# Kernel optimization log

Measured on AMD Instinct MI355X. Metric: run time of the kernel, lower is better.

Reference implementation:

```python
import jax, jax.numpy as jnp
import numpy as np

# ---- problem constants (match init_kwargs) ----
M, N, DV = 4096, 8192, 4   # checks, variables, column weight
SEED = 0
MAX_ITER = 10
ALPHA = 0.8
CLAMP = 20.0
BATCH = 256
PAD_BIG = 1.0e6


def _build_code():
    """Deterministic regular-column-weight LDPC pcm + padded adjacency (mirrors torch __init__)."""
    rng = np.random.default_rng(SEED)
    pcm = np.zeros((M, N), dtype=np.uint8)
    for v in range(N):
        checks = rng.choice(M, size=DV, replace=False)
        pcm[checks, v] = 1
    check_indices, var_indices = np.nonzero(pcm)  # row-major: sorted by check
    num_edges = len(check_indices)
    check_adj_lists = [[] for _ in range(M)]
    var_adj_lists = [[] for _ in range(N)]
    for e in range(num_edges):
        check_adj_lists[int(check_indices[e])].append(e)
        var_adj_lists[int(var_indices[e])].append(e)
    max_dc = max(len(a) for a in check_adj_lists)
    max_dv = max(len(a) for a in var_adj_lists)
    check_adj = np.zeros((M, max_dc), dtype=np.int64)
    check_mask = np.zeros((M, max_dc), dtype=np.float32)
    for c, adj in enumerate(check_adj_lists):
        for j, e in enumerate(adj):
            check_adj[c, j] = e
            check_mask[c, j] = 1.0
    var_adj = np.zeros((N, max_dv), dtype=np.int64)
    var_mask = np.zeros((N, max_dv), dtype=np.float32)
    for v, adj in enumerate(var_adj_lists):
        for j, e in enumerate(adj):
            var_adj[v, j] = e
            var_mask[v, j] = 1.0
    return pcm, check_indices, var_indices, check_adj, check_mask, var_adj, var_mask


def setup_inputs() -> dict:
    key = jax.random.key(0)
    k1, k2 = jax.random.split(key)
    pcm, _, var_idx, check_adj, check_mask, var_adj, var_mask = _build_code()
    syndrome = jax.random.randint(k1, (BATCH, M), 0, 2).astype(jnp.float32)
    channel_llr = jax.random.normal(k2, (BATCH, N), dtype=jnp.float32) * 2.0
    return {
        "syndrome": syndrome,
        "channel_llr": channel_llr,
        "var_adj": jnp.asarray(var_adj, jnp.int32),
        "var_adj_mask": jnp.asarray(var_mask),
        "check_adj": jnp.asarray(check_adj, jnp.int32),
        "check_adj_mask": jnp.asarray(check_mask),
        "var_idx": jnp.asarray(var_idx, jnp.int32),
        "pcm_dense": jnp.asarray(pcm, jnp.float32),
    }


def reference(syndrome, channel_llr, var_adj, var_adj_mask, check_adj, check_adj_mask, var_idx, pcm_dense):
    B = syndrome.shape[0]
    E = var_idx.shape[0]
    s_sign = 1.0 - 2.0 * syndrome                      # [B, m]
    flat_cidx = check_adj.reshape(-1)                  # [m*max_dc]; padded slots point to edge 0 with value 0

    def step(ctv, _):
        # variable-node update: gather check->var messages per variable
        var_total = jnp.sum(ctv[:, var_adj] * var_adj_mask, axis=2)           # [B, n]
        vtc = channel_llr[:, var_idx] + var_total[:, var_idx] - ctv           # [B, E]
        vtc = jnp.clip(vtc, -CLAMP, CLAMP)
        # check-node min-sum update
        vg = vtc[:, check_adj]                                                # [B, m, dc]
        signs = jnp.where(vg >= 0.0, 1.0, -1.0)                               # sign(0) -> +1, as in torch path
        signs_m = signs * check_adj_mask + (1.0 - check_adj_mask)             # padded -> +1
        total_sign = s_sign[:, :, None] * jnp.prod(signs_m, axis=2, keepdims=True)
        excl_sign = total_sign * signs_m                                      # divide == multiply for +/-1
        absv = jnp.abs(vg) + (1.0 - check_adj_mask) * PAD_BIG                 # [B, m, dc]
        neg_top2, _ = jax.lax.top_k(-absv, 2)                                 # two smallest magnitudes
        min1 = -neg_top2[..., 0:1]
        min2 = -neg_top2[..., 1:2]
        is_min = jnp.abs(absv - min1) < 1e-9
        excl_min = jnp.where(is_min, min2, min1)
        ctv_new = ALPHA * excl_sign * excl_min * check_adj_mask               # [B, m, dc]
        # scatter back to flat edge layout (each real edge written exactly once; padded values are 0)
        ctv = jnp.zeros((B, E), ctv.dtype).at[:, flat_cidx].add(ctv_new.reshape(B, -1))
        return ctv, None

    ctv0 = jnp.zeros((B, E), jnp.float32)
    ctv, _ = jax.lax.scan(step, ctv0, None, length=MAX_ITER)

    var_total = jnp.sum(ctv[:, var_adj] * var_adj_mask, axis=2)
    total_llr = channel_llr + var_total
    marginals = jax.nn.sigmoid(-total_llr)                                    # [B, n]
    hard_decision = (marginals > 0.5).astype(jnp.int32)
    syn_hat = jnp.mod(jnp.round(hard_decision.astype(jnp.float32) @ pcm_dense.T), 2.0)
    converged = jnp.sum(jnp.abs(syn_hat - syndrome), axis=1) < 0.5
    return marginals, hard_decision, converged
```

## Files before the change

kernel.cpp:

```cpp
#include <hip/hip_runtime.h>
#include <math.h>


#define BLOCK 1024
#define NV    8192
#define MC    4096
#define NE    32768
#define VPT   (NV / BLOCK)
#define CPT   (MC / BLOCK)
#define NITER 10
#define ALPHA 0.8f
#define CLAMP 20.0f
#define MSGW  40896
#define SGNB  0x80000000


__device__ __forceinline__ int pad_stride(int d) { return d + ((2 - (d & 3)) & 3); }

__global__ __launch_bounds__(BLOCK)
void setup_sort(const float* __restrict__ check_mask,
                const int*   __restrict__ check_adj,
                int max_dc, int* __restrict__ ws)
{
    __shared__ int hist[64], cbase[64], wsum[16];
    __shared__ int sdeg[MC];
    const int t = threadIdx.x;
    if (t < 64) hist[t] = 0;
    __syncthreads();
    int deg[CPT];
#pragma unroll
    for (int k = 0; k < CPT; ++k) {
        const int c = t + k * BLOCK;
        int d = 0;
        for (int j = 0; j < max_dc; ++j)
            d += (check_mask[(size_t)c * max_dc + j] != 0.0f) ? 1 : 0;
        deg[k] = d;
        atomicAdd(&hist[d & 63], 1);
    }
    __syncthreads();
    if (t == 0) {
        int s = 0;
        for (int i = 0; i < 64; ++i) { cbase[i] = s; s += hist[i]; }
    }
    __syncthreads();
#pragma unroll
    for (int k = 0; k < CPT; ++k) {
        const int pos = atomicAdd(&cbase[deg[k] & 63], 1);
        sdeg[pos]    = deg[k];
        ws[MC + pos] = t + k * BLOCK;
    }
    __syncthreads();
    int psz[CPT];
    int s = 0;
#pragma unroll
    for (int k = 0; k < CPT; ++k) {
        const int d = sdeg[4 * t + k];
        psz[k] = s;
        s += pad_stride(d);
    }
    const int lane = t & 63, wv = t >> 6;
    int run = s;
#pragma unroll
    for (int off = 1; off < 64; off <<= 1) {
        const int n = __shfl_up(run, off, 64);
        if (lane >= off) run += n;
    }
    if (lane == 63) wsum[wv] = run;
    __syncthreads();
    if (t == 0) {
        int acc = 0;
        for (int w = 0; w < 16; ++w) { const int v = wsum[w]; wsum[w] = acc; acc += v; }
    }
    __syncthreads();
    const int tb = wsum[wv] + (run - s);
#pragma unroll
    for (int k = 0; k < CPT; ++k) {
        const int i = 4 * t + k;
        ws[i] = ((tb + psz[k]) & 0xFFFF) | (sdeg[i] << 16);
    }
}

template<int D>
__device__ __forceinline__ void do_check_x(char* __restrict__ mb,
                                           int stB, int ssb, float pad)
{
    float x[D];
    constexpr int P = D / 2;
#pragma unroll
    for (int p = 0; p < P; ++p) {
        const float2 r = *(const float2*)(mb + stB + 8 * p);
        x[2 * p]     = r.x;
        x[2 * p + 1] = r.y;
    }
    if constexpr (D & 1)
        x[D - 1] = *(const float*)(mb + stB + 4 * (D - 1));

    float min1 = pad, min2 = pad;
    int sb = ssb;
#pragma unroll
    for (int j = 0; j < D; ++j) {
        sb ^= __float_as_int(x[j]);
        const float a = fabsf(x[j]);
        min2 = __builtin_amdgcn_fmed3f(min1, min2, a);
        min1 = fminf(min1, a);
    }
    const float vm1 = ALPHA * min1;
    const float vm2 = ALPHA * min2;
#pragma unroll
    for (int p = 0; p < P; ++p) {
        const int j0 = 2 * p, j1 = 2 * p + 1;
        const float m0 = (fabsf(fabsf(x[j0]) - min1) < 1e-9f) ? vm2 : vm1;
        const float m1 = (fabsf(fabsf(x[j1]) - min1) < 1e-9f) ? vm2 : vm1;
        float2 w;
        w.x = __int_as_float(__float_as_int(m0) | ((sb ^ __float_as_int(x[j0])) & SGNB));
        w.y = __int_as_float(__float_as_int(m1) | ((sb ^ __float_as_int(x[j1])) & SGNB));
        *(float2*)(mb + stB + 8 * p) = w;
    }
    if constexpr (D & 1) {
        const int jt = D - 1;
        const float mt = (fabsf(fabsf(x[jt]) - min1) < 1e-9f) ? vm2 : vm1;
        *(float*)(mb + stB + 4 * jt) =
            __int_as_float(__float_as_int(mt) | ((sb ^ __float_as_int(x[jt])) & SGNB));
    }
}

template<int DMAX>
__device__ __forceinline__ void do_check(char* __restrict__ mb,
                                         int stB, int d, int ssb, float pad)
{
    float x[DMAX];
    float min1 = pad, min2 = pad;
    int sb = ssb;
#pragma unroll
    for (int j = 0; j < DMAX; ++j) {
        if (j >= d) break;
        x[j] = *(const float*)(mb + stB + 4 * j);
    }
#pragma unroll
    for (int j = 0; j < DMAX; ++j) {
        if (j >= d) break;
        sb ^= __float_as_int(x[j]);
        const float a = fabsf(x[j]);
        min2 = __builtin_amdgcn_fmed3f(min1, min2, a);
        min1 = fminf(min1, a);
    }
    const float vm1 = ALPHA * min1;
    const float vm2 = ALPHA * min2;
#pragma unroll
    for (int j = 0; j < DMAX; ++j) {
        if (j >= d) break;
        const float m = (fabsf(fabsf(x[j]) - min1) < 1e-9f) ? vm2 : vm1;
        *(float*)(mb + stB + 4 * j) =
            __int_as_float(__float_as_int(m) | ((sb ^ __float_as_int(x[j])) & SGNB));
    }
}

__device__ void do_check_big(char* __restrict__ mb,
                             int stB, int d, int ssb, float pad)
{
    float min1 = pad, min2 = pad;
    int sb = ssb;
    for (int j = 0; j < d; ++j) {
        const float xx = *(const float*)(mb + stB + 4 * j);
        sb ^= __float_as_int(xx);
        const float aa = fabsf(xx);
        min2 = __builtin_amdgcn_fmed3f(min1, min2, aa);
        min1 = fminf(min1, aa);
    }
    const float vm1 = ALPHA * min1;
    const float vm2 = ALPHA * min2;
    for (int j = 0; j < d; ++j) {
        const float xx = *(const float*)(mb + stB + 4 * j);
        const float m  = (fabsf(fabsf(xx) - min1) < 1e-9f) ? vm2 : vm1;
        *(float*)(mb + stB + 4 * j) =
            __int_as_float(__float_as_int(m) | ((sb ^ __float_as_int(xx)) & SGNB));
    }
}

__device__ __forceinline__ void check_dispatch(char* __restrict__ mb,
                                               int stB, int d, int ssb, float pad)
{
    if      (d == 8)  do_check_x<8>(mb, stB, ssb, pad);
    else if (d == 7)  do_check_x<7>(mb, stB, ssb, pad);
    else if (d == 9)  do_check_x<9>(mb, stB, ssb, pad);
    else if (d == 6)  do_check_x<6>(mb, stB, ssb, pad);
    else if (d == 10) do_check_x<10>(mb, stB, ssb, pad);
    else if (d == 5)  do_check_x<5>(mb, stB, ssb, pad);
    else if (d == 11) do_check_x<11>(mb, stB, ssb, pad);
    else if (d == 12) do_check_x<12>(mb, stB, ssb, pad);
    else if (d == 4)  do_check_x<4>(mb, stB, ssb, pad);
    else if (d <= 3)  do_check<3>(mb, stB, d, ssb, pad);
    else if (d <= 16) do_check<16>(mb, stB, d, ssb, pad);
    else              do_check_big(mb, stB, d, ssb, pad);
}

__global__ __launch_bounds__(BLOCK) __attribute__((amdgpu_waves_per_eu(4, 4)))
void bp_decode(const float* __restrict__ syndrome,
               const float* __restrict__ llr_g,
               const int*   __restrict__ var_adj,
               const int*   __restrict__ var_idx,
               const int*   __restrict__ check_adj,
               int max_dc,
               const int*   __restrict__ ws,
               float* __restrict__ out,
               int B)
{
    __shared__ float msg[MSGW];
    __shared__ float sh_e0;
    __shared__ int   mism;

    const int b = blockIdx.x;
    const int t = threadIdx.x;
    char* mb = (char*)msg;

    int cstB[CPT], dsb[CPT];
    {
        int* posL = (int*)msg;
#pragma unroll
        for (int k = 0; k < CPT; ++k) {
            const int i = t + k * BLOCK;
            const int w = ws[i];
            const int c = ws[MC + i];
            const int pb = w & 0xFFFF;
            const int d  = w >> 16;
            cstB[k] = pb << 2;
            const int sb = (syndrome[(size_t)b * MC + c] > 0.5f) ? 1 : 0;
            dsb[k] = (d << 1) | sb;
            const int st = check_adj[(size_t)c * max_dc];
            for (int j = 0; j < d; ++j)
                posL[st + j] = pb + j;
        }
    }
    __syncthreads();

    const int  v0  = var_idx[0];
    const bool own = (t == (v0 & (BLOCK - 1)));
    const int  e0B = ((const int*)msg)[0] << 2;

    int   vsB[VPT][4];
    float llr[VPT];
    {
        const int* posL = (const int*)msg;
#pragma unroll
        for (int k = 0; k < VPT; ++k) {
            const int v = t + k * BLOCK;
            const int4 a = ((const int4*)var_adj)[v];
            vsB[k][0] = posL[a.x] << 2; vsB[k][1] = posL[a.y] << 2;
            vsB[k][2] = posL[a.z] << 2; vsB[k][3] = posL[a.w] << 2;
            llr[k] = llr_g[(size_t)b * NV + v];
        }
    }
    __syncthreads();

#pragma unroll
    for (int k = 0; k < VPT; ++k) {
        const float o = __builtin_amdgcn_fmed3f(llr[k], -CLAMP, CLAMP);
        *(float*)(mb + vsB[k][0]) = o;
        *(float*)(mb + vsB[k][1]) = o;
        *(float*)(mb + vsB[k][2]) = o;
        *(float*)(mb + vsB[k][3]) = o;
    }
    if (own) sh_e0 = fabsf(*(const float*)(mb + e0B)) + 1.0e6f;
    __syncthreads();
    {
        const float pad = sh_e0;
#pragma unroll
        for (int k = 0; k < CPT; ++k)
            check_dispatch(mb, cstB[k], dsb[k] >> 1, (dsb[k] & 1) << 31, pad);
    }
    __syncthreads();

#pragma unroll 1
    for (int it = 1; it < NITER; ++it) {
#pragma unroll
        for (int k = 0; k < VPT; ++k) {
            const float c0 = *(const float*)(mb + vsB[k][0]);
            const float c1 = *(const float*)(mb + vsB[k][1]);
            const float c2 = *(const float*)(mb + vsB[k][2]);
            const float c3 = *(const float*)(mb + vsB[k][3]);
            const float tot  = ((c0 + c1) + c2) + c3;
            const float bse  = llr[k] + tot;
            *(float*)(mb + vsB[k][0]) = __builtin_amdgcn_fmed3f(bse - c0, -CLAMP, CLAMP);
            *(float*)(mb + vsB[k][1]) = __builtin_amdgcn_fmed3f(bse - c1, -CLAMP, CLAMP);
            *(float*)(mb + vsB[k][2]) = __builtin_amdgcn_fmed3f(bse - c2, -CLAMP, CLAMP);
            *(float*)(mb + vsB[k][3]) = __builtin_amdgcn_fmed3f(bse - c3, -CLAMP, CLAMP);
        }
        if (own) sh_e0 = fabsf(*(const float*)(mb + e0B)) + 1.0e6f;
        __syncthreads();
        const float pad = sh_e0;

#pragma unroll
        for (int k = 0; k < CPT; ++k)
            check_dispatch(mb, cstB[k], dsb[k] >> 1, (dsb[k] & 1) << 31, pad);
        __syncthreads();
    }

    float marg[VPT], hard[VPT];
#pragma unroll
    for (int k = 0; k < VPT; ++k) {
        const float c0 = *(const float*)(mb + vsB[k][0]);
        const float c1 = *(const float*)(mb + vsB[k][1]);
        const float c2 = *(const float*)(mb + vsB[k][2]);
        const float c3 = *(const float*)(mb + vsB[k][3]);
        const float tot = ((c0 + c1) + c2) + c3;
        const float tl  = llr[k] + tot;
        const float mg  = 1.0f / (1.0f + expf(tl));
        marg[k] = mg;
        hard[k] = (mg > 0.5f) ? 1.0f : 0.0f;
    }
    if (t == 0) mism = 0;
    __syncthreads();

    const size_t BN = (size_t)B * NV;
#pragma unroll
    for (int k = 0; k < VPT; ++k) {
        const int v = t + k * BLOCK;
        out[(size_t)b * NV + v]      = marg[k];
        out[BN + (size_t)b * NV + v] = hard[k];
        const float h = hard[k];
        *(float*)(mb + vsB[k][0]) = h;
        *(float*)(mb + vsB[k][1]) = h;
        *(float*)(mb + vsB[k][2]) = h;
        *(float*)(mb + vsB[k][3]) = h;
    }
    __syncthreads();

#pragma unroll
    for (int k = 0; k < CPT; ++k) {
        const int d  = dsb[k] >> 1;
        const int sb = dsb[k] & 1;
        int par = 0;
        for (int j = 0; j < d; ++j)
            par ^= (*(const float*)(mb + cstB[k] + 4 * j) != 0.0f) ? 1 : 0;
        if (par != sb) mism = 1;
    }
    __syncthreads();
    if (t == 0) out[2 * BN + b] = mism ? 0.0f : 1.0f;
}

extern "C" void kernel_launch(void* const* d_in, const int* in_sizes, int n_in,
                              void* d_out, int out_size, void* d_ws, size_t ws_size,
                              hipStream_t stream) {
    const float* syndrome   = (const float*)d_in[0];
    const float* llr        = (const float*)d_in[1];
    const int*   var_adj    = (const int*)d_in[2];
    const int*   check_adj  = (const int*)d_in[4];
    const float* check_mask = (const float*)d_in[5];
    const int*   var_idx    = (const int*)d_in[6];
    float* out = (float*)d_out;
    int*   ws  = (int*)d_ws;

    const int B      = in_sizes[0] / MC;
    const int max_dc = in_sizes[4] / MC;

    setup_sort<<<1, BLOCK, 0, stream>>>(check_mask, check_adj, max_dc, ws);
    bp_decode<<<B, BLOCK, 0, stream>>>(syndrome, llr, var_adj, var_idx,
                                       check_adj, max_dc, ws, out, B);
}
```

Baseline: 334.9 us.

## Fold check degree sort into decode kernel, dropping separate setup launch

Removes the single-block setup_sort kernel and has every decode block recompute the check-degree counting sort and padded layout in shared memory. This eliminates a serialized single-block launch and the workspace round trip that precede the main decode. In exchange, each of the B blocks now redundantly reads the full check_mask and does shared-memory atomics before decoding.

```diff
diff --git a/kernel.cpp b/kernel.cpp
--- a/kernel.cpp
+++ b/kernel.cpp
@@ -14,71 +14,7 @@
 #define MSGW  40896
 #define SGNB  0x80000000
 
-
 __device__ __forceinline__ int pad_stride(int d) { return d + ((2 - (d & 3)) & 3); }
-
-__global__ __launch_bounds__(BLOCK)
-void setup_sort(const float* __restrict__ check_mask,
-                const int*   __restrict__ check_adj,
-                int max_dc, int* __restrict__ ws)
-{
-    __shared__ int hist[64], cbase[64], wsum[16];
-    __shared__ int sdeg[MC];
-    const int t = threadIdx.x;
-    if (t < 64) hist[t] = 0;
-    __syncthreads();
-    int deg[CPT];
-#pragma unroll
-    for (int k = 0; k < CPT; ++k) {
-        const int c = t + k * BLOCK;
-        int d = 0;
-        for (int j = 0; j < max_dc; ++j)
-            d += (check_mask[(size_t)c * max_dc + j] != 0.0f) ? 1 : 0;
-        deg[k] = d;
-        atomicAdd(&hist[d & 63], 1);
-    }
-    __syncthreads();
-    if (t == 0) {
-        int s = 0;
-        for (int i = 0; i < 64; ++i) { cbase[i] = s; s += hist[i]; }
-    }
-    __syncthreads();
-#pragma unroll
-    for (int k = 0; k < CPT; ++k) {
-        const int pos = atomicAdd(&cbase[deg[k] & 63], 1);
-        sdeg[pos]    = deg[k];
-        ws[MC + pos] = t + k * BLOCK;
-    }
-    __syncthreads();
-    int psz[CPT];
-    int s = 0;
-#pragma unroll
-    for (int k = 0; k < CPT; ++k) {
-        const int d = sdeg[4 * t + k];
-        psz[k] = s;
-        s += pad_stride(d);
-    }
-    const int lane = t & 63, wv = t >> 6;
-    int run = s;
-#pragma unroll
-    for (int off = 1; off < 64; off <<= 1) {
-        const int n = __shfl_up(run, off, 64);
-        if (lane >= off) run += n;
-    }
-    if (lane == 63) wsum[wv] = run;
-    __syncthreads();
-    if (t == 0) {
-        int acc = 0;
-        for (int w = 0; w < 16; ++w) { const int v = wsum[w]; wsum[w] = acc; acc += v; }
-    }
-    __syncthreads();
-    const int tb = wsum[wv] + (run - s);
-#pragma unroll
-    for (int k = 0; k < CPT; ++k) {
-        const int i = 4 * t + k;
-        ws[i] = ((tb + psz[k]) & 0xFFFF) | (sdeg[i] << 16);
-    }
-}
 
 template<int D>
 __device__ __forceinline__ void do_check_x(char* __restrict__ mb,
@@ -200,8 +136,8 @@
                const int*   __restrict__ var_adj,
                const int*   __restrict__ var_idx,
                const int*   __restrict__ check_adj,
+               const float* __restrict__ check_mask,
                int max_dc,
-               const int*   __restrict__ ws,
                float* __restrict__ out,
                int B)
 {
@@ -212,43 +148,96 @@
     const int b = blockIdx.x;
     const int t = threadIdx.x;
     char* mb = (char*)msg;
-
-    int cstB[CPT], dsb[CPT];
+    int* arena = (int*)msg;
+
+    int* degL = arena;
+    int* bins = arena + MC;
+    int* rec1 = arena + MC + 64;
+    int* rec2 = arena + 2 * MC + 64;
+
+    for (int i = t; i < MC + 64; i += BLOCK) arena[i] = 0;
+    __syncthreads();
+
     {
-        int* posL = (int*)msg;
-#pragma unroll
-        for (int k = 0; k < CPT; ++k) {
-            const int i = t + k * BLOCK;
-            const int w = ws[i];
-            const int c = ws[MC + i];
-            const int pb = w & 0xFFFF;
-            const int d  = w >> 16;
-            cstB[k] = pb << 2;
-            const int sb = (syndrome[(size_t)b * MC + c] > 0.5f) ? 1 : 0;
-            dsb[k] = (d << 1) | sb;
-            const int st = check_adj[(size_t)c * max_dc];
-            for (int j = 0; j < d; ++j)
-                posL[st + j] = pb + j;
+        const int total = MC * max_dc;
+        const int qs = BLOCK / max_dc, rs = BLOCK % max_dc;
+        int c = t / max_dc, j = t % max_dc;
+        for (int e = t; e < total; e += BLOCK) {
+            if (check_mask[e] != 0.0f) atomicAdd(&degL[c], 1);
+            c += qs; j += rs;
+            if (j >= max_dc) { j -= max_dc; ++c; }
         }
+    }
+    __syncthreads();
+
+    int myd[CPT];
+#pragma unroll
+    for (int k = 0; k < CPT; ++k) {
+        myd[k] = degL[t + k * BLOCK] & 63;
+        atomicAdd(&bins[myd[k]], 1);
+    }
+    __syncthreads();
+
+    if (t == 0) {
+        int cs = 0, ps = 0;
+        for (int d = 0; d < 64; ++d) {
+            const int cnt = bins[d];
+            bins[d] = (cs & 0xFFFF) | (ps << 16);
+            cs += cnt;
+            ps += cnt * pad_stride(d);
+        }
+    }
+    __syncthreads();
+
+#pragma unroll
+    for (int k = 0; k < CPT; ++k) {
+        const int c = t + k * BLOCK;
+        const int d = myd[k];
+        const int old = atomicAdd(&bins[d], 1 | (pad_stride(d) << 16));
+        const int pos = old & 0xFFFF;
+        const int pb  = (old >> 16) & 0xFFFF;
+        rec1[pos] = pb | (d << 16);
+        rec2[pos] = c;
+    }
+    __syncthreads();
+
+    int cstB[CPT], dsb[CPT], stE[CPT];
+#pragma unroll
+    for (int k = 0; k < CPT; ++k) {
+        const int i = t + k * BLOCK;
+        const int w = rec1[i];
+        const int c = rec2[i];
+        cstB[k] = (w & 0xFFFF) << 2;
+        const int d  = w >> 16;
+        const int sb = (syndrome[(size_t)b * MC + c] > 0.5f) ? 1 : 0;
+        dsb[k] = (d << 1) | sb;
+        stE[k] = check_adj[(size_t)c * max_dc];
+    }
+    __syncthreads();
+
+#pragma unroll
+    for (int k = 0; k < CPT; ++k) {
+        const int d  = dsb[k] >> 1;
+        const int pb = cstB[k] >> 2;
+        const int st = stE[k];
+        for (int j = 0; j < d; ++j)
+            arena[st + j] = pb + j;
     }
     __syncthreads();
 
     const int  v0  = var_idx[0];
     const bool own = (t == (v0 & (BLOCK - 1)));
-    const int  e0B = ((const int*)msg)[0] << 2;
+    const int  e0B = arena[0] << 2;
 
     int   vsB[VPT][4];
     float llr[VPT];
-    {
-        const int* posL = (const int*)msg;
-#pragma unroll
-        for (int k = 0; k < VPT; ++k) {
-            const int v = t + k * BLOCK;
-            const int4 a = ((const int4*)var_adj)[v];
-            vsB[k][0] = posL[a.x] << 2; vsB[k][1] = posL[a.y] << 2;
-            vsB[k][2] = posL[a.z] << 2; vsB[k][3] = posL[a.w] << 2;
-            llr[k] = llr_g[(size_t)b * NV + v];
-        }
+#pragma unroll
+    for (int k = 0; k < VPT; ++k) {
+        const int v = t + k * BLOCK;
+        const int4 a = ((const int4*)var_adj)[v];
+        vsB[k][0] = arena[a.x] << 2; vsB[k][1] = arena[a.y] << 2;
+        vsB[k][2] = arena[a.z] << 2; vsB[k][3] = arena[a.w] << 2;
+        llr[k] = llr_g[(size_t)b * NV + v];
     }
     __syncthreads();
 
@@ -348,12 +337,11 @@
     const float* check_mask = (const float*)d_in[5];
     const int*   var_idx    = (const int*)d_in[6];
     float* out = (float*)d_out;
-    int*   ws  = (int*)d_ws;
+    (void)d_ws; (void)ws_size;
 
     const int B      = in_sizes[0] / MC;
     const int max_dc = in_sizes[4] / MC;
 
-    setup_sort<<<1, BLOCK, 0, stream>>>(check_mask, check_adj, max_dc, ws);
     bp_decode<<<B, BLOCK, 0, stream>>>(syndrome, llr, var_adj, var_idx,
-                                       check_adj, max_dc, ws, out, B);
-}
+                                       check_adj, check_mask, max_dc, out, B);
+}
```

Result: slower. 356.1 us (+6.3%).
